# Optimization experiments

Hardware: AMD Instinct MI355X
Metric: run time of the kernel (lower is better)

Reference implementation:

```python
import jax, jax.numpy as jnp
import numpy as np

B, C, L = 2048, 9605, 8
ALPHA = 0.5        # self.alpha
ALPHA1 = 0.05      # margin
ALPHA2 = 2.0       # asymmetric scale when violated
ALPHA3 = 5.0       # logistic sharpness
ALPHA_OTHER = 0.3  # floor on top-k threshold
TOPK = 16          # x_sorted[15] -> 16th largest


def setup_inputs() -> dict:
    key = jax.random.key(0)
    k1, k2, k3, k4 = jax.random.split(key, 4)
    x = jax.random.normal(k1, (B, C), dtype=jnp.float32)
    # each class assigned to one of 5*L slots; slots < L are whitelist groups,
    # the rest are 'other' classes (like total_indices in the torch code)
    gid = jax.random.randint(k4, (C,), 0, 5 * L)
    gid = gid.at[:L].set(jnp.arange(L))  # guarantee every group is non-empty
    group_mask = gid[None, :] == jnp.arange(L)[:, None]  # [L, C] bool
    # sparse multi-label binarized targets (~14 positives/sample)
    y = (jax.random.uniform(k2, (B, C)) < 0.0015).astype(jnp.float32)
    y_neg = (jax.random.uniform(k3, (B, C)) < 0.0015).astype(jnp.float32)
    return {"x": x, "y": y, "y_neg": y_neg, "group_mask": group_mask}


def _rank_loss(x1, x2):
    # our_rank_loss: sigmoid(alpha3*(x2-x1+margin)), scaled by alpha2 when violated
    d = x2 - x1 + ALPHA1
    s = jax.nn.sigmoid(ALPHA3 * d)
    return jnp.where(d > 0, ALPHA2 * s, s)


def reference(x, y, y_neg, group_mask):
    xs = jax.nn.sigmoid(x)  # [B, C]
    # top_k_thres = max(16th-largest sigmoid score, alpha_other)
    thres = jnp.maximum(jax.lax.top_k(xs, TOPK)[0][:, TOPK - 1], ALPHA_OTHER)  # [B]
    maskf = group_mask.astype(xs.dtype)  # [L, C]
    neg_inf = jnp.array(-jnp.inf, xs.dtype)
    # per-sample max score inside each whitelist group: [B, L]
    group_max = jnp.max(jnp.where(group_mask[None, :, :], xs[:, None, :], neg_inf), axis=-1)
    # find_gt_whitelist: group is 'hit' if any positive target inside it
    gt = (y @ maskf.T) > 0        # [B, L]
    gt_neg = (y_neg @ maskf.T) > 0  # [B, L]
    has_gt = jnp.any(gt, axis=-1)    # [B]; False <=> sentinel len(all_labels)
    has_neg = jnp.any(gt_neg, axis=-1)
    # ---- case B: sample hits at least one whitelist group ----
    rl_correct = _rank_loss(group_max, thres[:, None])    # gt groups above thres
    rl_incorrect = _rank_loss(thres[:, None], group_max)  # non-gt groups below thres
    caseB = jnp.sum(jnp.where(gt, rl_correct, rl_incorrect), axis=-1)  # [B]
    # ---- case A: no whitelist group hit ----
    union = jnp.any(group_mask, axis=0)  # [C] union of all whitelist classes
    union_max = jnp.max(jnp.where(union[None, :], xs, neg_inf), axis=-1)  # [B]
    neg_max = jnp.max(jnp.where(gt_neg, group_max, neg_inf), axis=-1)
    neg_score = jnp.where(has_neg, neg_max, jnp.zeros((), xs.dtype))  # torch starts at 0
    caseA = (1.0 - ALPHA) * _rank_loss(thres, union_max) + ALPHA * _rank_loss(thres, neg_score)
    loss_rank_all = jnp.where(has_gt, caseB, caseA)  # [B]
    return jnp.mean(loss_rank_all)
```

## Files before the change

kernel.cpp:

```cpp
#include <hip/hip_runtime.h>
#include <math.h>

constexpr int B_ = 2048;
constexpr int C_ = 9605;
constexpr int L_ = 8;
constexpr int TOPK_ = 16;
constexpr int CAPQ_ = 512;
constexpr float T0_ = 2.0f;
constexpr int CPAD_ = 9728;

__device__ __forceinline__ float sigm(float v) { return 1.0f / (1.0f + expf(-v)); }

__device__ __forceinline__ float rank_loss(float x1, float x2) {
  float d = x2 - x1 + 0.05f;
  float s = 1.0f / (1.0f + expf(-5.0f * d));
  return (d > 0.0f) ? 2.0f * s : s;
}

__device__ __forceinline__ unsigned int fkey(float v) {
  unsigned int u = __float_as_uint(v);
  return u ^ ((u & 0x80000000u) ? 0xFFFFFFFFu : 0x80000000u);
}
__device__ __forceinline__ float fkeyinv(unsigned int k) {
  unsigned int u = (k & 0x80000000u) ? (k ^ 0x80000000u) : ~k;
  return __uint_as_float(u);
}

__global__ void build_code_kernel(const int* __restrict__ mask,
                                  unsigned char* __restrict__ code) {
  int c = blockIdx.x * 256 + threadIdx.x;
  if (c >= CPAD_) return;
  unsigned char cd = 0xFF;
  if (c < C_) {
#pragma unroll
    for (int l = L_ - 1; l >= 0; --l)
      if (mask[l * C_ + c] != 0) cd = (unsigned char)l;
  }
  code[c] = cd;
}

__global__ void __launch_bounds__(256, 8) row_loss_kernel(
    const float* __restrict__ x, const float* __restrict__ y,
    const float* __restrict__ yn, const unsigned char* __restrict__ code,
    float* __restrict__ loss) {
  __shared__ unsigned int lds_code[2404];
  __shared__ float4 cand4[CAPQ_];
  __shared__ unsigned int gslot[L_];
  __shared__ int cand_cnt;
  __shared__ unsigned int gt_bits, gtn_bits;
  __shared__ float s_x16;
  __shared__ int s_flag, s_red;

  const int t = threadIdx.x;
  const int b = blockIdx.x;
  const float* xr = x + (size_t)b * C_;
  const float* yr = y + (size_t)b * C_;
  const float* ynr = yn + (size_t)b * C_;

  const int lead = (4 - ((b * C_) & 3)) & 3;
  const int n4 = (C_ - lead) >> 2;

  if (t < L_) gslot[t] = 0x80000000u;
  if (t == 0) { cand_cnt = 0; gt_bits = 0u; gtn_bits = 0u; s_flag = 0; }

  const unsigned int* cdw = (const unsigned int*)code;
  if (lead == 0) {
    for (int j = t; j < n4; j += 256) lds_code[j] = cdw[j];
  } else {
    const int sh = lead << 3;
    for (int j = t; j < n4; j += 256) {
      unsigned int d0 = cdw[j], d1 = cdw[j + 1];
      lds_code[j] = (d0 >> sh) | (d1 << (32 - sh));
    }
  }
  __syncthreads();

  auto LDQ = [&](int jq, float4& X, float4& Y, float4& N) {
    int js = (jq < n4) ? jq : 0;
    int c0 = lead + (js << 2);
    X = *reinterpret_cast<const float4*>(xr + c0);
    Y = *reinterpret_cast<const float4*>(yr + c0);
    N = *reinterpret_cast<const float4*>(ynr + c0);
  };

  auto PROC = [&](const float4& X, const float4& Y, const float4& N, int jx) {
    if (jx >= n4) return;
    unsigned int cw = lds_code[jx];
    float mx = fmaxf(fmaxf(X.x, X.y), fmaxf(X.z, X.w));
    if (mx > T0_) {
      int p = atomicAdd(&cand_cnt, 1);
      if (p < CAPQ_) cand4[p] = X;
    }
    unsigned int cd;
    cd = cw & 0xFFu;
    if (cd < 8u && X.x > 0.0f) atomicMax(&gslot[cd], __float_as_uint(X.x) | 0x80000000u);
    cd = (cw >> 8) & 0xFFu;
    if (cd < 8u && X.y > 0.0f) atomicMax(&gslot[cd], __float_as_uint(X.y) | 0x80000000u);
    cd = (cw >> 16) & 0xFFu;
    if (cd < 8u && X.z > 0.0f) atomicMax(&gslot[cd], __float_as_uint(X.z) | 0x80000000u);
    cd = cw >> 24;
    if (cd < 8u && X.w > 0.0f) atomicMax(&gslot[cd], __float_as_uint(X.w) | 0x80000000u);
    float sy = Y.x + Y.y + Y.z + Y.w + N.x + N.y + N.z + N.w;
    if (sy > 0.0f) {
      if (Y.x > 0.0f || N.x > 0.0f) { unsigned int d = cw & 0xFFu;        if (d < 8u) { if (Y.x > 0.0f) atomicOr(&gt_bits, 1u << d); if (N.x > 0.0f) atomicOr(&gtn_bits, 1u << d); } }
      if (Y.y > 0.0f || N.y > 0.0f) { unsigned int d = (cw >> 8) & 0xFFu; if (d < 8u) { if (Y.y > 0.0f) atomicOr(&gt_bits, 1u << d); if (N.y > 0.0f) atomicOr(&gtn_bits, 1u << d); } }
      if (Y.z > 0.0f || N.z > 0.0f) { unsigned int d = (cw >> 16) & 0xFFu;if (d < 8u) { if (Y.z > 0.0f) atomicOr(&gt_bits, 1u << d); if (N.z > 0.0f) atomicOr(&gtn_bits, 1u << d); } }
      if (Y.w > 0.0f || N.w > 0.0f) { unsigned int d = cw >> 24;          if (d < 8u) { if (Y.w > 0.0f) atomicOr(&gt_bits, 1u << d); if (N.w > 0.0f) atomicOr(&gtn_bits, 1u << d); } }
    }
  };

  float4 xa, ya, na, xb, yb, nb, xc, yc, nc;
  int ja = t, jb = t + 256, jc = t + 512, jn = t + 768;
  LDQ(ja, xa, ya, na);
  LDQ(jb, xb, yb, nb);
  LDQ(jc, xc, yc, nc);
#pragma unroll
  for (int base = 0; base < 3; ++base) {
    PROC(xa, ya, na, ja); LDQ(jn, xa, ya, na); ja = jn; jn += 256;
    PROC(xb, yb, nb, jb); LDQ(jn, xb, yb, nb); jb = jn; jn += 256;
    PROC(xc, yc, nc, jc); LDQ(jn, xc, yc, nc); jc = jn; jn += 256;
  }
  PROC(xa, ya, na, ja);

  if (t < 4) {
    auto sc = [&](int c) {
      float xv = xr[c], yv = yr[c], nv = ynr[c];
      unsigned int cd = code[c];
      if (cd < 8u) {
        if (xv > 0.0f) atomicMax(&gslot[cd], __float_as_uint(xv) | 0x80000000u);
        if (yv > 0.0f) atomicOr(&gt_bits, 1u << cd);
        if (nv > 0.0f) atomicOr(&gtn_bits, 1u << cd);
      }
      if (xv > T0_) {
        int p = atomicAdd(&cand_cnt, 1);
        if (p < CAPQ_) cand4[p] = make_float4(xv, -INFINITY, -INFINITY, -INFINITY);
      }
    };
    if (t < lead) sc(t);
    int c2 = lead + (n4 << 2) + t;
    if (c2 < C_) sc(c2);
  }
  __syncthreads();

  const int qn = cand_cnt;
  const bool ok_path = (qn >= 4) && (qn <= CAPQ_);
  if (ok_path && t < 64) {
    const float* cf = reinterpret_cast<const float*>(cand4);
    const int nvv = qn << 2;
    unsigned int ku[32];
#pragma unroll
    for (int k = 0; k < 32; ++k) {
      int i = t + (k << 6);
      ku[k] = (i < nvv) ? fkey(cf[i]) : 0u;
    }
    unsigned int lo = 0u, hi = 0xFFFFFFFFu;
#pragma unroll 1
    for (int it = 0; it < 32 && lo < hi; ++it) {
      unsigned int mid = lo + ((hi - lo) >> 1) + 1u;
      int c16 = 0;
#pragma unroll
      for (int k = 0; k < 32; ++k) c16 += (ku[k] >= mid) ? 1 : 0;
#pragma unroll
      for (int off = 32; off > 0; off >>= 1) c16 += __shfl_xor(c16, off, 64);
      if (c16 >= TOPK_) lo = mid; else hi = mid - 1u;
    }
    if (t == 0) {
      float v = fkeyinv(lo);
      s_x16 = v;
      s_flag = (v > T0_) ? 1 : 0;
    }
  }
  __syncthreads();
  if (!(ok_path && s_flag != 0)) {
    unsigned int lo = 0u, hi = 0xFFFFFFFFu;
    for (int it = 0; it < 32; ++it) {
      if (lo >= hi) break;
      unsigned int mid = lo + ((hi - lo) >> 1) + 1u;
      if (t == 0) s_red = 0;
      __syncthreads();
      int cl = 0;
      for (int c = t; c < C_; c += 256) cl += (fkey(xr[c]) >= mid) ? 1 : 0;
      atomicAdd(&s_red, cl);
      __syncthreads();
      int total = s_red;
      __syncthreads();
      if (total >= TOPK_) lo = mid; else hi = mid - 1u;
    }
    if (t == 0) s_x16 = fkeyinv(lo);
  }
  __syncthreads();

  if (t == 0) {
    float thres = fmaxf(sigm(s_x16), 0.3f);
    unsigned int gtb = gt_bits, gnb = gtn_bits;
    float caseB = 0.0f, unio = -INFINITY, negmax = -INFINITY;
#pragma unroll
    for (int l = 0; l < L_; ++l) {
      float gm = __uint_as_float(gslot[l] ^ 0x80000000u);
      float g = sigm(gm);
      unio = fmaxf(unio, g);
      caseB += ((gtb >> l) & 1u) ? rank_loss(g, thres) : rank_loss(thres, g);
      if ((gnb >> l) & 1u) negmax = fmaxf(negmax, g);
    }
    float negscore = (gnb != 0u) ? negmax : 0.0f;
    float caseA = 0.5f * rank_loss(thres, unio) + 0.5f * rank_loss(thres, negscore);
    loss[b] = (gtb != 0u) ? caseB : caseA;
  }
}

__global__ void mean_kernel(const float* __restrict__ loss, float* __restrict__ out) {
  const int t = threadIdx.x;
  float s = 0.0f;
  for (int i = t; i < B_; i += 256) s += loss[i];
#pragma unroll
  for (int off = 32; off > 0; off >>= 1) s += __shfl_xor(s, off, 64);
  __shared__ float part[4];
  if ((t & 63) == 0) part[t >> 6] = s;
  __syncthreads();
  if (t == 0) out[0] = (part[0] + part[1] + part[2] + part[3]) * (1.0f / (float)B_);
}

extern "C" void kernel_launch(void* const* d_in, const int* in_sizes, int n_in,
                              void* d_out, int out_size, void* d_ws, size_t ws_size,
                              hipStream_t stream) {
  const float* x = (const float*)d_in[0];
  const float* y = (const float*)d_in[1];
  const float* yn = (const float*)d_in[2];
  const int* mask = (const int*)d_in[3];

  float* loss = (float*)d_ws;
  unsigned char* code = (unsigned char*)d_ws + B_ * sizeof(float);

  hipLaunchKernelGGL(build_code_kernel, dim3((CPAD_ + 255) / 256), dim3(256), 0, stream,
                     mask, code);
  hipLaunchKernelGGL(row_loss_kernel, dim3(B_), dim3(256), 0, stream,
                     x, y, yn, code, loss);
  hipLaunchKernelGGL(mean_kernel, dim3(1), dim3(256), 0, stream,
                     loss, (float*)d_out);
}
```

Measured before the change: 256.4 us.

## Use 512-thread blocks, inline-asm loads with manual waitcnt, and skip redundant LDS atomics

The row kernel moves from 256 to 512 threads per block. The three input streams are now fetched with inline-asm global_load_dwordx4 and a double-buffered schedule, with an explicit vmcnt wait before each chunk is processed. The group-max and label-bit updates now read shared memory first and issue the atomic only when it would change the value, which is meant to cut LDS atomic contention. In exchange, the correctness of the hand-written waitcnt counts depends on no other vector-memory operations slipping in between, and the 4-per-CU launch bound may limit register allocation.

```diff
diff --git a/kernel.cpp b/kernel.cpp
--- a/kernel.cpp
+++ b/kernel.cpp
@@ -39,7 +39,7 @@
   code[c] = cd;
 }
 
-__global__ void __launch_bounds__(256, 8) row_loss_kernel(
+__global__ void __launch_bounds__(512, 4) row_loss_kernel(
     const float* __restrict__ x, const float* __restrict__ y,
     const float* __restrict__ yn, const unsigned char* __restrict__ code,
     float* __restrict__ loss) {
@@ -53,78 +53,101 @@
 
   const int t = threadIdx.x;
   const int b = blockIdx.x;
-  const float* xr = x + (size_t)b * C_;
-  const float* yr = y + (size_t)b * C_;
-  const float* ynr = yn + (size_t)b * C_;
-
   const int lead = (4 - ((b * C_) & 3)) & 3;
   const int n4 = (C_ - lead) >> 2;
 
+  const float* xb = x + (size_t)(b * C_ + lead);
+  const float* yb = y + (size_t)(b * C_ + lead);
+  const float* nb = yn + (size_t)(b * C_ + lead);
+
   if (t < L_) gslot[t] = 0x80000000u;
   if (t == 0) { cand_cnt = 0; gt_bits = 0u; gtn_bits = 0u; s_flag = 0; }
 
   const unsigned int* cdw = (const unsigned int*)code;
   if (lead == 0) {
-    for (int j = t; j < n4; j += 256) lds_code[j] = cdw[j];
+    for (int j = t; j < n4; j += 512) lds_code[j] = cdw[j];
   } else {
     const int sh = lead << 3;
-    for (int j = t; j < n4; j += 256) {
+    for (int j = t; j < n4; j += 512) {
       unsigned int d0 = cdw[j], d1 = cdw[j + 1];
       lds_code[j] = (d0 >> sh) | (d1 << (32 - sh));
     }
   }
   __syncthreads();
 
-  auto LDQ = [&](int jq, float4& X, float4& Y, float4& N) {
-    int js = (jq < n4) ? jq : 0;
-    int c0 = lead + (js << 2);
-    X = *reinterpret_cast<const float4*>(xr + c0);
-    Y = *reinterpret_cast<const float4*>(yr + c0);
-    N = *reinterpret_cast<const float4*>(ynr + c0);
+  float4 XA, YA, NA, XB, YB, NB;
+
+  auto ISSUE = [&](int j, float4& X, float4& Y, float4& N) {
+    int js = (j < n4) ? j : 0;
+    unsigned int vo = (unsigned int)js << 4;
+    asm volatile("global_load_dwordx4 %0, %1, %2" : "=v"(X) : "v"(vo), "s"(xb));
+    asm volatile("global_load_dwordx4 %0, %1, %2" : "=v"(Y) : "v"(vo), "s"(yb));
+    asm volatile("global_load_dwordx4 %0, %1, %2" : "=v"(N) : "v"(vo), "s"(nb));
   };
 
-  auto PROC = [&](const float4& X, const float4& Y, const float4& N, int jx) {
-    if (jx >= n4) return;
-    unsigned int cw = lds_code[jx];
+  auto PROC = [&](const float4& X, const float4& Y, const float4& N, int j) {
+    if (j >= n4) return;
+    unsigned int cw = lds_code[j];
     float mx = fmaxf(fmaxf(X.x, X.y), fmaxf(X.z, X.w));
     if (mx > T0_) {
       int p = atomicAdd(&cand_cnt, 1);
       if (p < CAPQ_) cand4[p] = X;
     }
-    unsigned int cd;
-    cd = cw & 0xFFu;
-    if (cd < 8u && X.x > 0.0f) atomicMax(&gslot[cd], __float_as_uint(X.x) | 0x80000000u);
-    cd = (cw >> 8) & 0xFFu;
-    if (cd < 8u && X.y > 0.0f) atomicMax(&gslot[cd], __float_as_uint(X.y) | 0x80000000u);
-    cd = (cw >> 16) & 0xFFu;
-    if (cd < 8u && X.z > 0.0f) atomicMax(&gslot[cd], __float_as_uint(X.z) | 0x80000000u);
-    cd = cw >> 24;
-    if (cd < 8u && X.w > 0.0f) atomicMax(&gslot[cd], __float_as_uint(X.w) | 0x80000000u);
+    {
+      unsigned int cd, k;
+      cd = cw & 0xFFu;
+      if (cd < 8u && X.x > 0.0f) { k = __float_as_uint(X.x) | 0x80000000u; if (k > gslot[cd]) atomicMax(&gslot[cd], k); }
+      cd = (cw >> 8) & 0xFFu;
+      if (cd < 8u && X.y > 0.0f) { k = __float_as_uint(X.y) | 0x80000000u; if (k > gslot[cd]) atomicMax(&gslot[cd], k); }
+      cd = (cw >> 16) & 0xFFu;
+      if (cd < 8u && X.z > 0.0f) { k = __float_as_uint(X.z) | 0x80000000u; if (k > gslot[cd]) atomicMax(&gslot[cd], k); }
+      cd = cw >> 24;
+      if (cd < 8u && X.w > 0.0f) { k = __float_as_uint(X.w) | 0x80000000u; if (k > gslot[cd]) atomicMax(&gslot[cd], k); }
+    }
     float sy = Y.x + Y.y + Y.z + Y.w + N.x + N.y + N.z + N.w;
     if (sy > 0.0f) {
-      if (Y.x > 0.0f || N.x > 0.0f) { unsigned int d = cw & 0xFFu;        if (d < 8u) { if (Y.x > 0.0f) atomicOr(&gt_bits, 1u << d); if (N.x > 0.0f) atomicOr(&gtn_bits, 1u << d); } }
-      if (Y.y > 0.0f || N.y > 0.0f) { unsigned int d = (cw >> 8) & 0xFFu; if (d < 8u) { if (Y.y > 0.0f) atomicOr(&gt_bits, 1u << d); if (N.y > 0.0f) atomicOr(&gtn_bits, 1u << d); } }
-      if (Y.z > 0.0f || N.z > 0.0f) { unsigned int d = (cw >> 16) & 0xFFu;if (d < 8u) { if (Y.z > 0.0f) atomicOr(&gt_bits, 1u << d); if (N.z > 0.0f) atomicOr(&gtn_bits, 1u << d); } }
-      if (Y.w > 0.0f || N.w > 0.0f) { unsigned int d = cw >> 24;          if (d < 8u) { if (Y.w > 0.0f) atomicOr(&gt_bits, 1u << d); if (N.w > 0.0f) atomicOr(&gtn_bits, 1u << d); } }
+      unsigned int d;
+      d = cw & 0xFFu;
+      if (d < 8u) { if (Y.x > 0.0f && !((gt_bits >> d) & 1u)) atomicOr(&gt_bits, 1u << d); if (N.x > 0.0f && !((gtn_bits >> d) & 1u)) atomicOr(&gtn_bits, 1u << d); }
+      d = (cw >> 8) & 0xFFu;
+      if (d < 8u) { if (Y.y > 0.0f && !((gt_bits >> d) & 1u)) atomicOr(&gt_bits, 1u << d); if (N.y > 0.0f && !((gtn_bits >> d) & 1u)) atomicOr(&gtn_bits, 1u << d); }
+      d = (cw >> 16) & 0xFFu;
+      if (d < 8u) { if (Y.z > 0.0f && !((gt_bits >> d) & 1u)) atomicOr(&gt_bits, 1u << d); if (N.z > 0.0f && !((gtn_bits >> d) & 1u)) atomicOr(&gtn_bits, 1u << d); }
+      d = cw >> 24;
+      if (d < 8u) { if (Y.w > 0.0f && !((gt_bits >> d) & 1u)) atomicOr(&gt_bits, 1u << d); if (N.w > 0.0f && !((gtn_bits >> d) & 1u)) atomicOr(&gtn_bits, 1u << d); }
     }
   };
 
-  float4 xa, ya, na, xb, yb, nb, xc, yc, nc;
-  int ja = t, jb = t + 256, jc = t + 512, jn = t + 768;
-  LDQ(ja, xa, ya, na);
-  LDQ(jb, xb, yb, nb);
-  LDQ(jc, xc, yc, nc);
-#pragma unroll
-  for (int base = 0; base < 3; ++base) {
-    PROC(xa, ya, na, ja); LDQ(jn, xa, ya, na); ja = jn; jn += 256;
-    PROC(xb, yb, nb, jb); LDQ(jn, xb, yb, nb); jb = jn; jn += 256;
-    PROC(xc, yc, nc, jc); LDQ(jn, xc, yc, nc); jc = jn; jn += 256;
-  }
-  PROC(xa, ya, na, ja);
+  ISSUE(t, XA, YA, NA);
+  ISSUE(t + 512, XB, YB, NB);
+
+  asm volatile("s_waitcnt vmcnt(3)" ::: "memory");
+  __builtin_amdgcn_sched_barrier(0);
+  PROC(XA, YA, NA, t);
+  ISSUE(t + 1024, XA, YA, NA);
+
+  asm volatile("s_waitcnt vmcnt(3)" ::: "memory");
+  __builtin_amdgcn_sched_barrier(0);
+  PROC(XB, YB, NB, t + 512);
+  ISSUE(t + 1536, XB, YB, NB);
+
+  asm volatile("s_waitcnt vmcnt(3)" ::: "memory");
+  __builtin_amdgcn_sched_barrier(0);
+  PROC(XA, YA, NA, t + 1024);
+  ISSUE(t + 2048, XA, YA, NA);
+
+  asm volatile("s_waitcnt vmcnt(3)" ::: "memory");
+  __builtin_amdgcn_sched_barrier(0);
+  PROC(XB, YB, NB, t + 1536);
+
+  asm volatile("s_waitcnt vmcnt(0)" ::: "memory");
+  __builtin_amdgcn_sched_barrier(0);
+  PROC(XA, YA, NA, t + 2048);
 
   if (t < 4) {
     auto sc = [&](int c) {
-      float xv = xr[c], yv = yr[c], nv = ynr[c];
+      float xv = x[(size_t)b * C_ + c], yv = y[(size_t)b * C_ + c],
+            nv = yn[(size_t)b * C_ + c];
       unsigned int cd = code[c];
       if (cd < 8u) {
         if (xv > 0.0f) atomicMax(&gslot[cd], __float_as_uint(xv) | 0x80000000u);
@@ -172,6 +195,7 @@
   }
   __syncthreads();
   if (!(ok_path && s_flag != 0)) {
+    const float* xr = x + (size_t)b * C_;
     unsigned int lo = 0u, hi = 0xFFFFFFFFu;
     for (int it = 0; it < 32; ++it) {
       if (lo >= hi) break;
@@ -179,7 +203,7 @@
       if (t == 0) s_red = 0;
       __syncthreads();
       int cl = 0;
-      for (int c = t; c < C_; c += 256) cl += (fkey(xr[c]) >= mid) ? 1 : 0;
+      for (int c = t; c < C_; c += 512) cl += (fkey(xr[c]) >= mid) ? 1 : 0;
       atomicAdd(&s_red, cl);
       __syncthreads();
       int total = s_red;
@@ -231,9 +255,9 @@
   float* loss = (float*)d_ws;
   unsigned char* code = (unsigned char*)d_ws + B_ * sizeof(float);
 
-  hipLaunchKernelGGL(build_code_kernel, dim3((CPAD_ + 255) / 256), dim3(256), 0, stream,
-                     mask, code);
-  hipLaunchKernelGGL(row_loss_kernel, dim3(B_), dim3(256), 0, stream,
+  hipLaunchKernelGGL(build_code_kernel, dim3((CPAD_ + 255) / 256), dim3(256), 0,
+                     stream, mask, code);
+  hipLaunchKernelGGL(row_loss_kernel, dim3(B_), dim3(512), 0, stream,
                      x, y, yn, code, loss);
   hipLaunchKernelGGL(mean_kernel, dim3(1), dim3(256), 0, stream,
                      loss, (float*)d_out);
```

New measurement: 257.1 us. No clear change (+0.3%).

## Split per-row work into separate x/y/yneg blocks with per-thread group slots

Applied to the files above, without the earlier changes.

Splits each row's work across three blocks: one processes x (group max and top-k candidates), and the other two reduce y or y_neg into group bitmasks. A separate finish kernel then combines the partial results. Four pre-shifted copies of the code array remove the per-block LDS code staging, and per-thread private slots with a tree reduction replace contended shared atomicMax. The candidate cap is lowered to 384. This raises the block count to spread the memory traffic, at the cost of an extra kernel launch, extra global intermediates, and more fallback risk if a row has more candidates than the smaller cap.

```diff
diff --git a/kernel.cpp b/kernel.cpp
--- a/kernel.cpp
+++ b/kernel.cpp
@@ -5,9 +5,9 @@
 constexpr int C_ = 9605;
 constexpr int L_ = 8;
 constexpr int TOPK_ = 16;
-constexpr int CAPQ_ = 512;
+constexpr int CAPQ_ = 384;
 constexpr float T0_ = 2.0f;
-constexpr int CPAD_ = 9728;
+constexpr int CS_ = 9632;
 
 __device__ __forceinline__ float sigm(float v) { return 1.0f / (1.0f + expf(-v)); }
 
@@ -26,186 +26,221 @@
   return __uint_as_float(u);
 }
 
-__global__ void build_code_kernel(const int* __restrict__ mask,
-                                  unsigned char* __restrict__ code) {
-  int c = blockIdx.x * 256 + threadIdx.x;
-  if (c >= CPAD_) return;
-  unsigned char cd = 0xFF;
-  if (c < C_) {
-#pragma unroll
-    for (int l = L_ - 1; l >= 0; --l)
-      if (mask[l * C_ + c] != 0) cd = (unsigned char)l;
+__global__ void setup_kernel(const int* __restrict__ mask,
+                             unsigned char* __restrict__ code4,
+                             unsigned int* __restrict__ gtG,
+                             unsigned int* __restrict__ gtnG) {
+  const int tid = blockIdx.x * 256 + threadIdx.x;
+  if (tid < CS_ + 3) {
+    unsigned char cd = 0xFF;
+    if (tid < C_) {
+#pragma unroll
+      for (int l = L_ - 1; l >= 0; --l)
+        if (mask[l * C_ + tid] != 0) cd = (unsigned char)l;
+    }
+#pragma unroll
+    for (int ld = 0; ld < 4; ++ld) {
+      int p = tid - ld;
+      if (p >= 0 && p < CS_) code4[ld * CS_ + p] = cd;
+    }
   }
-  code[c] = cd;
-}
-
-__global__ void __launch_bounds__(256, 8) row_loss_kernel(
+  if (tid < B_) { gtG[tid] = 0u; gtnG[tid] = 0u; }
+}
+
+__global__ void __launch_bounds__(256, 8) rows3_kernel(
     const float* __restrict__ x, const float* __restrict__ y,
-    const float* __restrict__ yn, const unsigned char* __restrict__ code,
-    float* __restrict__ loss) {
-  __shared__ unsigned int lds_code[2404];
+    const float* __restrict__ yn, const unsigned char* __restrict__ code4,
+    unsigned int* __restrict__ gslotG, unsigned int* __restrict__ gtG,
+    unsigned int* __restrict__ gtnG, float* __restrict__ x16G) {
+  __shared__ unsigned int slots[256 * 9];
   __shared__ float4 cand4[CAPQ_];
-  __shared__ unsigned int gslot[L_];
-  __shared__ int cand_cnt;
-  __shared__ unsigned int gt_bits, gtn_bits;
+  __shared__ int cnt;
   __shared__ float s_x16;
   __shared__ int s_flag, s_red;
-
+  __shared__ unsigned int wb[4];
+
+  const int g = (int)blockIdx.x >> 11;
+  const int r = (int)blockIdx.x & 2047;
   const int t = threadIdx.x;
-  const int b = blockIdx.x;
-  const float* xr = x + (size_t)b * C_;
-  const float* yr = y + (size_t)b * C_;
-  const float* ynr = yn + (size_t)b * C_;
-
-  const int lead = (4 - ((b * C_) & 3)) & 3;
+  const int lead = (4 - ((r * C_) & 3)) & 3;
   const int n4 = (C_ - lead) >> 2;
-
-  if (t < L_) gslot[t] = 0x80000000u;
-  if (t == 0) { cand_cnt = 0; gt_bits = 0u; gtn_bits = 0u; s_flag = 0; }
-
-  const unsigned int* cdw = (const unsigned int*)code;
-  if (lead == 0) {
-    for (int j = t; j < n4; j += 256) lds_code[j] = cdw[j];
+  const size_t rowb = (size_t)r * C_;
+
+  if (g == 0) {
+#pragma unroll
+    for (int i = 0; i < 9; ++i) slots[t * 9 + i] = 0u;
+    if (t == 0) { cnt = 0; s_flag = 0; }
+    __syncthreads();
+
+    const float* xb = x + rowb + lead;
+    const unsigned int* cb = (const unsigned int*)(code4 + (size_t)lead * CS_);
+
+#pragma unroll
+    for (int k = 0; k < 10; ++k) {
+      const int j = t + (k << 8);
+      if (j < n4) {
+        float4 X = *reinterpret_cast<const float4*>(xb + (j << 2));
+        unsigned int cw = cb[j];
+        {
+          unsigned int k0 = (X.x > 0.0f) ? (__float_as_uint(X.x) | 0x80000000u) : 0u;
+          unsigned int k1 = (X.y > 0.0f) ? (__float_as_uint(X.y) | 0x80000000u) : 0u;
+          unsigned int k2 = (X.z > 0.0f) ? (__float_as_uint(X.z) | 0x80000000u) : 0u;
+          unsigned int k3 = (X.w > 0.0f) ? (__float_as_uint(X.w) | 0x80000000u) : 0u;
+          unsigned int a0 = min(cw & 0xFFu, 8u);
+          unsigned int a1 = min((cw >> 8) & 0xFFu, 8u);
+          unsigned int a2 = min((cw >> 16) & 0xFFu, 8u);
+          unsigned int a3 = min(cw >> 24, 8u);
+          atomicMax(&slots[t * 9 + a0], k0);
+          atomicMax(&slots[t * 9 + a1], k1);
+          atomicMax(&slots[t * 9 + a2], k2);
+          atomicMax(&slots[t * 9 + a3], k3);
+        }
+        float mx = fmaxf(fmaxf(X.x, X.y), fmaxf(X.z, X.w));
+        if (mx > T0_) {
+          int p = atomicAdd(&cnt, 1);
+          if (p < CAPQ_) cand4[p] = X;
+        }
+      }
+    }
+
+    if (t < 4) {
+      auto sc = [&](int c) {
+        float xv = x[rowb + c];
+        unsigned int cd = code4[c];
+        unsigned int key = (xv > 0.0f) ? (__float_as_uint(xv) | 0x80000000u) : 0u;
+        atomicMax(&slots[t * 9 + min(cd, 8u)], key);
+        if (xv > T0_) {
+          int p = atomicAdd(&cnt, 1);
+          if (p < CAPQ_) cand4[p] = make_float4(xv, -INFINITY, -INFINITY, -INFINITY);
+        }
+      };
+      if (t < lead) sc(t);
+      int c2 = lead + (n4 << 2) + t;
+      if (c2 < C_) sc(c2);
+    }
+    __syncthreads();
+
+    for (int s = 128; s > 0; s >>= 1) {
+      if (t < s) {
+#pragma unroll
+        for (int l = 0; l < 8; ++l) {
+          unsigned int o = slots[(t + s) * 9 + l];
+          if (o > slots[t * 9 + l]) slots[t * 9 + l] = o;
+        }
+      }
+      __syncthreads();
+    }
+    if (t < 8) gslotG[r * 8 + t] = slots[t];
+
+    const int qn = cnt;
+    const bool ok_path = (qn >= 4) && (qn <= CAPQ_);
+    if (ok_path && t < 64) {
+      const float* cf = reinterpret_cast<const float*>(cand4);
+      const int nvv = qn << 2;
+      unsigned int ku[CAPQ_ * 4 / 64];
+#pragma unroll
+      for (int k = 0; k < CAPQ_ * 4 / 64; ++k) {
+        int i = t + (k << 6);
+        ku[k] = (i < nvv) ? fkey(cf[i]) : 0u;
+      }
+      unsigned int lo = 0u, hi = 0xFFFFFFFFu;
+#pragma unroll 1
+      for (int it = 0; it < 32 && lo < hi; ++it) {
+        unsigned int mid = lo + ((hi - lo) >> 1) + 1u;
+        int c16 = 0;
+#pragma unroll
+        for (int k = 0; k < CAPQ_ * 4 / 64; ++k) c16 += (ku[k] >= mid) ? 1 : 0;
+#pragma unroll
+        for (int off = 32; off > 0; off >>= 1) c16 += __shfl_xor(c16, off, 64);
+        if (c16 >= TOPK_) lo = mid; else hi = mid - 1u;
+      }
+      if (t == 0) {
+        float v = fkeyinv(lo);
+        s_x16 = v;
+        s_flag = (v > T0_) ? 1 : 0;
+      }
+    }
+    __syncthreads();
+    if (!(ok_path && s_flag != 0)) {
+      const float* xr = x + rowb;
+      unsigned int lo = 0u, hi = 0xFFFFFFFFu;
+      for (int it = 0; it < 32; ++it) {
+        if (lo >= hi) break;
+        unsigned int mid = lo + ((hi - lo) >> 1) + 1u;
+        if (t == 0) s_red = 0;
+        __syncthreads();
+        int cl = 0;
+        for (int c = t; c < C_; c += 256) cl += (fkey(xr[c]) >= mid) ? 1 : 0;
+        atomicAdd(&s_red, cl);
+        __syncthreads();
+        int total = s_red;
+        __syncthreads();
+        if (total >= TOPK_) lo = mid; else hi = mid - 1u;
+      }
+      if (t == 0) s_x16 = fkeyinv(lo);
+    }
+    __syncthreads();
+    if (t == 0) x16G[r] = s_x16;
   } else {
-    const int sh = lead << 3;
-    for (int j = t; j < n4; j += 256) {
-      unsigned int d0 = cdw[j], d1 = cdw[j + 1];
-      lds_code[j] = (d0 >> sh) | (d1 << (32 - sh));
-    }
+    const float* src = (g == 1) ? y : yn;
+    unsigned int* dst = (g == 1) ? gtG : gtnG;
+    const float* sb = src + rowb + lead;
+    unsigned int bits = 0u;
+
+#pragma unroll
+    for (int k = 0; k < 10; ++k) {
+      const int j = t + (k << 8);
+      if (j < n4) {
+        float4 V = *reinterpret_cast<const float4*>(sb + (j << 2));
+        if (V.x > 0.0f || V.y > 0.0f || V.z > 0.0f || V.w > 0.0f) {
+          int c = lead + (j << 2);
+          if (V.x > 0.0f) { unsigned int cd = code4[c];     if (cd < 8u) bits |= 1u << cd; }
+          if (V.y > 0.0f) { unsigned int cd = code4[c + 1]; if (cd < 8u) bits |= 1u << cd; }
+          if (V.z > 0.0f) { unsigned int cd = code4[c + 2]; if (cd < 8u) bits |= 1u << cd; }
+          if (V.w > 0.0f) { unsigned int cd = code4[c + 3]; if (cd < 8u) bits |= 1u << cd; }
+        }
+      }
+    }
+    if (t < 4) {
+      if (t < lead) {
+        float v = src[rowb + t];
+        if (v > 0.0f) { unsigned int cd = code4[t]; if (cd < 8u) bits |= 1u << cd; }
+      }
+      int c2 = lead + (n4 << 2) + t;
+      if (c2 < C_) {
+        float v = src[rowb + c2];
+        if (v > 0.0f) { unsigned int cd = code4[c2]; if (cd < 8u) bits |= 1u << cd; }
+      }
+    }
+#pragma unroll
+    for (int off = 32; off > 0; off >>= 1) bits |= __shfl_xor(bits, off, 64);
+    if ((t & 63) == 0) wb[t >> 6] = bits;
+    __syncthreads();
+    if (t == 0) dst[r] = wb[0] | wb[1] | wb[2] | wb[3];
   }
-  __syncthreads();
-
-  auto LDQ = [&](int jq, float4& X, float4& Y, float4& N) {
-    int js = (jq < n4) ? jq : 0;
-    int c0 = lead + (js << 2);
-    X = *reinterpret_cast<const float4*>(xr + c0);
-    Y = *reinterpret_cast<const float4*>(yr + c0);
-    N = *reinterpret_cast<const float4*>(ynr + c0);
-  };
-
-  auto PROC = [&](const float4& X, const float4& Y, const float4& N, int jx) {
-    if (jx >= n4) return;
-    unsigned int cw = lds_code[jx];
-    float mx = fmaxf(fmaxf(X.x, X.y), fmaxf(X.z, X.w));
-    if (mx > T0_) {
-      int p = atomicAdd(&cand_cnt, 1);
-      if (p < CAPQ_) cand4[p] = X;
-    }
-    unsigned int cd;
-    cd = cw & 0xFFu;
-    if (cd < 8u && X.x > 0.0f) atomicMax(&gslot[cd], __float_as_uint(X.x) | 0x80000000u);
-    cd = (cw >> 8) & 0xFFu;
-    if (cd < 8u && X.y > 0.0f) atomicMax(&gslot[cd], __float_as_uint(X.y) | 0x80000000u);
-    cd = (cw >> 16) & 0xFFu;
-    if (cd < 8u && X.z > 0.0f) atomicMax(&gslot[cd], __float_as_uint(X.z) | 0x80000000u);
-    cd = cw >> 24;
-    if (cd < 8u && X.w > 0.0f) atomicMax(&gslot[cd], __float_as_uint(X.w) | 0x80000000u);
-    float sy = Y.x + Y.y + Y.z + Y.w + N.x + N.y + N.z + N.w;
-    if (sy > 0.0f) {
-      if (Y.x > 0.0f || N.x > 0.0f) { unsigned int d = cw & 0xFFu;        if (d < 8u) { if (Y.x > 0.0f) atomicOr(&gt_bits, 1u << d); if (N.x > 0.0f) atomicOr(&gtn_bits, 1u << d); } }
-      if (Y.y > 0.0f || N.y > 0.0f) { unsigned int d = (cw >> 8) & 0xFFu; if (d < 8u) { if (Y.y > 0.0f) atomicOr(&gt_bits, 1u << d); if (N.y > 0.0f) atomicOr(&gtn_bits, 1u << d); } }
-      if (Y.z > 0.0f || N.z > 0.0f) { unsigned int d = (cw >> 16) & 0xFFu;if (d < 8u) { if (Y.z > 0.0f) atomicOr(&gt_bits, 1u << d); if (N.z > 0.0f) atomicOr(&gtn_bits, 1u << d); } }
-      if (Y.w > 0.0f || N.w > 0.0f) { unsigned int d = cw >> 24;          if (d < 8u) { if (Y.w > 0.0f) atomicOr(&gt_bits, 1u << d); if (N.w > 0.0f) atomicOr(&gtn_bits, 1u << d); } }
-    }
-  };
-
-  float4 xa, ya, na, xb, yb, nb, xc, yc, nc;
-  int ja = t, jb = t + 256, jc = t + 512, jn = t + 768;
-  LDQ(ja, xa, ya, na);
-  LDQ(jb, xb, yb, nb);
-  LDQ(jc, xc, yc, nc);
-#pragma unroll
-  for (int base = 0; base < 3; ++base) {
-    PROC(xa, ya, na, ja); LDQ(jn, xa, ya, na); ja = jn; jn += 256;
-    PROC(xb, yb, nb, jb); LDQ(jn, xb, yb, nb); jb = jn; jn += 256;
-    PROC(xc, yc, nc, jc); LDQ(jn, xc, yc, nc); jc = jn; jn += 256;
+}
+
+__global__ void finish_kernel(const unsigned int* __restrict__ gslotG,
+                              const unsigned int* __restrict__ gtG,
+                              const unsigned int* __restrict__ gtnG,
+                              const float* __restrict__ x16G,
+                              float* __restrict__ loss) {
+  const int r = blockIdx.x * 256 + threadIdx.x;
+  if (r >= B_) return;
+  float thres = fmaxf(sigm(x16G[r]), 0.3f);
+  unsigned int gtb = gtG[r], gnb = gtnG[r];
+  float caseB = 0.0f, unio = -INFINITY, negmax = -INFINITY;
+#pragma unroll
+  for (int l = 0; l < L_; ++l) {
+    float gm = __uint_as_float(gslotG[r * L_ + l] ^ 0x80000000u);
+    float g = sigm(gm);
+    unio = fmaxf(unio, g);
+    caseB += ((gtb >> l) & 1u) ? rank_loss(g, thres) : rank_loss(thres, g);
+    if ((gnb >> l) & 1u) negmax = fmaxf(negmax, g);
   }
-  PROC(xa, ya, na, ja);
-
-  if (t < 4) {
-    auto sc = [&](int c) {
-      float xv = xr[c], yv = yr[c], nv = ynr[c];
-      unsigned int cd = code[c];
-      if (cd < 8u) {
-        if (xv > 0.0f) atomicMax(&gslot[cd], __float_as_uint(xv) | 0x80000000u);
-        if (yv > 0.0f) atomicOr(&gt_bits, 1u << cd);
-        if (nv > 0.0f) atomicOr(&gtn_bits, 1u << cd);
-      }
-      if (xv > T0_) {
-        int p = atomicAdd(&cand_cnt, 1);
-        if (p < CAPQ_) cand4[p] = make_float4(xv, -INFINITY, -INFINITY, -INFINITY);
-      }
-    };
-    if (t < lead) sc(t);
-    int c2 = lead + (n4 << 2) + t;
-    if (c2 < C_) sc(c2);
-  }
-  __syncthreads();
-
-  const int qn = cand_cnt;
-  const bool ok_path = (qn >= 4) && (qn <= CAPQ_);
-  if (ok_path && t < 64) {
-    const float* cf = reinterpret_cast<const float*>(cand4);
-    const int nvv = qn << 2;
-    unsigned int ku[32];
-#pragma unroll
-    for (int k = 0; k < 32; ++k) {
-      int i = t + (k << 6);
-      ku[k] = (i < nvv) ? fkey(cf[i]) : 0u;
-    }
-    unsigned int lo = 0u, hi = 0xFFFFFFFFu;
-#pragma unroll 1
-    for (int it = 0; it < 32 && lo < hi; ++it) {
-      unsigned int mid = lo + ((hi - lo) >> 1) + 1u;
-      int c16 = 0;
-#pragma unroll
-      for (int k = 0; k < 32; ++k) c16 += (ku[k] >= mid) ? 1 : 0;
-#pragma unroll
-      for (int off = 32; off > 0; off >>= 1) c16 += __shfl_xor(c16, off, 64);
-      if (c16 >= TOPK_) lo = mid; else hi = mid - 1u;
-    }
-    if (t == 0) {
-      float v = fkeyinv(lo);
-      s_x16 = v;
-      s_flag = (v > T0_) ? 1 : 0;
-    }
-  }
-  __syncthreads();
-  if (!(ok_path && s_flag != 0)) {
-    unsigned int lo = 0u, hi = 0xFFFFFFFFu;
-    for (int it = 0; it < 32; ++it) {
-      if (lo >= hi) break;
-      unsigned int mid = lo + ((hi - lo) >> 1) + 1u;
-      if (t == 0) s_red = 0;
-      __syncthreads();
-      int cl = 0;
-      for (int c = t; c < C_; c += 256) cl += (fkey(xr[c]) >= mid) ? 1 : 0;
-      atomicAdd(&s_red, cl);
-      __syncthreads();
-      int total = s_red;
-      __syncthreads();
-      if (total >= TOPK_) lo = mid; else hi = mid - 1u;
-    }
-    if (t == 0) s_x16 = fkeyinv(lo);
-  }
-  __syncthreads();
-
-  if (t == 0) {
-    float thres = fmaxf(sigm(s_x16), 0.3f);
-    unsigned int gtb = gt_bits, gnb = gtn_bits;
-    float caseB = 0.0f, unio = -INFINITY, negmax = -INFINITY;
-#pragma unroll
-    for (int l = 0; l < L_; ++l) {
-      float gm = __uint_as_float(gslot[l] ^ 0x80000000u);
-      float g = sigm(gm);
-      unio = fmaxf(unio, g);
-      caseB += ((gtb >> l) & 1u) ? rank_loss(g, thres) : rank_loss(thres, g);
-      if ((gnb >> l) & 1u) negmax = fmaxf(negmax, g);
-    }
-    float negscore = (gnb != 0u) ? negmax : 0.0f;
-    float caseA = 0.5f * rank_loss(thres, unio) + 0.5f * rank_loss(thres, negscore);
-    loss[b] = (gtb != 0u) ? caseB : caseA;
-  }
+  float negscore = (gnb != 0u) ? negmax : 0.0f;
+  float caseA = 0.5f * rank_loss(thres, unio) + 0.5f * rank_loss(thres, negscore);
+  loss[r] = (gtb != 0u) ? caseB : caseA;
 }
 
 __global__ void mean_kernel(const float* __restrict__ loss, float* __restrict__ out) {
@@ -228,13 +263,26 @@
   const float* yn = (const float*)d_in[2];
   const int* mask = (const int*)d_in[3];
 
-  float* loss = (float*)d_ws;
-  unsigned char* code = (unsigned char*)d_ws + B_ * sizeof(float);
-
-  hipLaunchKernelGGL(build_code_kernel, dim3((CPAD_ + 255) / 256), dim3(256), 0, stream,
-                     mask, code);
-  hipLaunchKernelGGL(row_loss_kernel, dim3(B_), dim3(256), 0, stream,
-                     x, y, yn, code, loss);
+  constexpr size_t OFF_LOSS = 0;
+  constexpr size_t OFF_CODE4 = 8192;
+  constexpr size_t OFF_GSLOT = OFF_CODE4 + 4 * CS_;
+  constexpr size_t OFF_GT = OFF_GSLOT + B_ * L_ * 4;
+  constexpr size_t OFF_GTN = OFF_GT + B_ * 4;
+  constexpr size_t OFF_X16 = OFF_GTN + B_ * 4;
+
+  float* loss = (float*)((char*)d_ws + OFF_LOSS);
+  unsigned char* code4 = (unsigned char*)d_ws + OFF_CODE4;
+  unsigned int* gslotG = (unsigned int*)((char*)d_ws + OFF_GSLOT);
+  unsigned int* gtG = (unsigned int*)((char*)d_ws + OFF_GT);
+  unsigned int* gtnG = (unsigned int*)((char*)d_ws + OFF_GTN);
+  float* x16G = (float*)((char*)d_ws + OFF_X16);
+
+  hipLaunchKernelGGL(setup_kernel, dim3(38), dim3(256), 0, stream,
+                     mask, code4, gtG, gtnG);
+  hipLaunchKernelGGL(rows3_kernel, dim3(3 * B_), dim3(256), 0, stream,
+                     x, y, yn, code4, gslotG, gtG, gtnG, x16G);
+  hipLaunchKernelGGL(finish_kernel, dim3((B_ + 255) / 256), dim3(256), 0, stream,
+                     gslotG, gtG, gtnG, x16G, loss);
   hipLaunchKernelGGL(mean_kernel, dim3(1), dim3(256), 0, stream,
                      loss, (float*)d_out);
 }
```

Measured after the change: 254.8 us. Within noise of the previous version (-0.6%).
